# Performance work log

Hardware: AMD Instinct MI355X
Metric: run time of the kernel (lower is better)

The kernel has to match this reference:

```python
import jax, jax.numpy as jnp
import numpy as np

HEADS = 16


def setup_inputs() -> dict:
    key0 = jax.random.key(0)
    ks = jax.random.split(key0, 12)
    B, S, H = 4, 2048, 1024
    init = lambda k, shape: (jax.random.normal(k, shape, dtype=jnp.float32) * 0.02)
    return {
        "key": jax.random.normal(ks[0], (B, S, H), dtype=jnp.float32),
        "query": jax.random.normal(ks[1], (B, S, H), dtype=jnp.float32),
        "value": jax.random.normal(ks[2], (B, S, H), dtype=jnp.float32),
        "mask": jnp.zeros((B, 1, S, S), dtype=jnp.float32),  # additive mask
        "wq": init(ks[3], (H, H)), "bq": jnp.zeros((H,), jnp.float32),
        "wk": init(ks[4], (H, H)), "bk": jnp.zeros((H,), jnp.float32),
        "wv": init(ks[5], (H, H)), "bv": jnp.zeros((H,), jnp.float32),
        "wo": init(ks[6], (H, H)), "bo": jnp.zeros((H,), jnp.float32),
    }


def reference(key, query, value, mask, wq, bq, wk, bk, wv, bv, wo, bo):
    B, S, H = query.shape
    Hs = H // HEADS
    # Linear projections (torch Linear: x @ W^T + b), split heads -> [B, Hn, S, Hs]
    split = lambda x: x.reshape(B, S, HEADS, Hs).transpose(0, 2, 1, 3)
    q = split(query @ wq.T + bq)
    k = split(key @ wk.T + bk)
    v = split(value @ wv.T + bv)
    scale = 1.0 / jnp.sqrt(jnp.asarray(Hs, q.dtype))
    scores = jnp.einsum("bhqd,bhkd->bhqk", q, k) * scale  # [B, Hn, S, S]
    probs = jax.nn.softmax(scores + mask, axis=-1)  # dropout p=0 -> identity
    ctx = jnp.einsum("bhqk,bhkd->bhqd", probs, v)
    ctx = ctx.transpose(0, 2, 1, 3).reshape(B, S, H)
    return ctx @ wo.T + bo
```

## Files before the change

kernel.cpp:

```cpp
#include <hip/hip_runtime.h>
#include <hip/hip_bf16.h>

typedef __bf16 bf16;
typedef __bf16 bf16x4 __attribute__((ext_vector_type(4)));
typedef __bf16 bf16x8 __attribute__((ext_vector_type(8)));
typedef float f32x4 __attribute__((ext_vector_type(4)));
typedef float f32x16 __attribute__((ext_vector_type(16)));
typedef unsigned u32x4 __attribute__((ext_vector_type(4)));

#define MFMA16(a, b, c) __builtin_amdgcn_mfma_f32_16x16x32_bf16((a), (b), (c), 0, 0, 0)
#define MFMA32(a, b, c) __builtin_amdgcn_mfma_f32_32x32x16_bf16((a), (b), (c), 0, 0, 0)

__device__ __forceinline__ int xcd_swizzle(int bid, int nblk) {
  const int per = nblk >> 3;
  return (bid & 7) * per + (bid >> 3);
}

__device__ __forceinline__ void gload_lds16(const bf16* g, bf16* lds) {
  __builtin_amdgcn_global_load_lds(
      (const __attribute__((address_space(1))) void*)g,
      (__attribute__((address_space(3))) void*)lds, 16, 0, 0);
}

__device__ __forceinline__ float fast_exp2(float x) {
  float r;
  asm("v_exp_f32 %0, %1\n\ts_nop 1" : "=v"(r) : "v"(x));
  return r;
}

__device__ __forceinline__ unsigned cvt_pk_bf16(float lo, float hi) {
  unsigned r;
  asm("v_cvt_pk_bf16_f32 %0, %1, %2" : "=v"(r) : "v"(lo), "v"(hi));
  return r;
}

template <typename T> struct StageRegs;
template <> struct StageRegs<float> { float4 lo[2], hi[2]; };
template <> struct StageRegs<bf16> { bf16x8 v[2]; };

template <typename T>
__device__ __forceinline__ void stage_issue(StageRegs<T>& r, const T* base,
                                            int brc, int k0, int tid) {
#pragma unroll
  for (int i = 0; i < 2; ++i) {
    const int c = i * 256 + tid;
    const int row = c >> 2, lin = c & 3;
    const T* p = base + (size_t)(brc + row) * 1024 + k0 + lin * 8;
    if constexpr (sizeof(T) == 4) {
      r.lo[i] = *reinterpret_cast<const float4*>(p);
      r.hi[i] = *reinterpret_cast<const float4*>(p + 4);
    } else {
      r.v[i] = *reinterpret_cast<const bf16x8*>(p);
    }
  }
}

template <typename T>
__device__ __forceinline__ void stage_write(const StageRegs<T>& r, bf16* sm,
                                            int tid) {
#pragma unroll
  for (int i = 0; i < 2; ++i) {
    const int c = i * 256 + tid;
    const int row = c >> 2, lin = c & 3;
    const int slot = lin ^ (row & 3);
    if constexpr (sizeof(T) == 4) {
      const float4 a = r.lo[i], b = r.hi[i];
      u32x4 w;
      w[0] = cvt_pk_bf16(a.x, a.y);
      w[1] = cvt_pk_bf16(a.z, a.w);
      w[2] = cvt_pk_bf16(b.x, b.y);
      w[3] = cvt_pk_bf16(b.z, b.w);
      *reinterpret_cast<u32x4*>(sm + row * 32 + slot * 8) = w;
    } else {
      *reinterpret_cast<bf16x8*>(sm + row * 32 + slot * 8) = r.v[i];
    }
  }
}

template <typename TA>
__device__ __forceinline__ void gemm_core(const TA* A, const float* W,
                                          int brow, int bcol, int tid, int wm,
                                          int wn, int l15, int l4,
                                          bf16 (*Asm)[4096], bf16 (*Bsm)[4096],
                                          f32x4 (&acc)[4][4]) {
  StageRegs<TA> ra;
  StageRegs<float> rb;
  stage_issue(ra, A, brow, 0, tid);
  stage_issue(rb, W, bcol, 0, tid);
  int p = 0;
  for (int t = 0; t < 32; ++t) {
    stage_write(ra, Asm[p], tid);
    stage_write(rb, Bsm[p], tid);
    __syncthreads();
    if (t + 1 < 32) {
      stage_issue(ra, A, brow, (t + 1) << 5, tid);
      stage_issue(rb, W, bcol, (t + 1) << 5, tid);
    }
    bf16x8 af[4], bfr[4];
#pragma unroll
    for (int m = 0; m < 4; ++m) {
      const int row = wm + m * 16 + l15;
      const int slot = l4 ^ (row & 3);
      af[m] = *reinterpret_cast<const bf16x8*>(Asm[p] + row * 32 + slot * 8);
    }
#pragma unroll
    for (int n = 0; n < 4; ++n) {
      const int row = wn + n * 16 + l15;
      const int slot = l4 ^ (row & 3);
      bfr[n] = *reinterpret_cast<const bf16x8*>(Bsm[p] + row * 32 + slot * 8);
    }
    __builtin_amdgcn_s_setprio(1);
#pragma unroll
    for (int m = 0; m < 4; ++m)
#pragma unroll
      for (int n = 0; n < 4; ++n)
        acc[m][n] = MFMA16(af[m], bfr[n], acc[m][n]);
    __builtin_amdgcn_s_setprio(0);
    p ^= 1;
  }
}

__global__ __launch_bounds__(256, 2) void qkv_gemm_kernel(
    const float* __restrict__ query, const float* __restrict__ key,
    const float* __restrict__ value, const float* __restrict__ wq,
    const float* __restrict__ wk, const float* __restrict__ wv,
    const float* __restrict__ bq, const float* __restrict__ bk,
    const float* __restrict__ bv, bf16* __restrict__ Qws,
    bf16* __restrict__ Kws, bf16* __restrict__ Vt, float qscale) {
  __shared__ bf16 Asm[2][128 * 32];
  __shared__ bf16 Bsm[2][128 * 32];
  const int tid = threadIdx.x;
  const int lane = tid & 63;
  const int wid = tid >> 6;
  const int l15 = lane & 15;
  const int l4 = lane >> 4;
  const int bid = xcd_swizzle(blockIdx.x, 1536);
  const int seg = bid / 512;
  const int inner = bid % 512;
  const int brow = (inner >> 3) << 7;
  const int bcol = (inner & 7) << 7;
  const int wm = (wid >> 1) << 6;
  const int wn = (wid & 1) << 6;

  const float* A = seg == 0 ? query : (seg == 1 ? key : value);
  const float* W = seg == 0 ? wq : (seg == 1 ? wk : wv);
  const float* bias = seg == 0 ? bq : (seg == 1 ? bk : bv);

  f32x4 acc[4][4] = {};
  gemm_core(A, W, brow, bcol, tid, wm, wn, l15, l4, Asm, Bsm, acc);

  const int r0 = brow + wm + l4 * 4;
  const int c0 = bcol + wn + l15;
  if (seg < 2) {
    bf16* C = seg == 0 ? Qws : Kws;
    const float cs = seg == 0 ? qscale : 1.0f;
#pragma unroll
    for (int n = 0; n < 4; ++n) {
      const float bvv = bias[c0 + n * 16];
#pragma unroll
      for (int m = 0; m < 4; ++m)
#pragma unroll
        for (int r = 0; r < 4; ++r)
          C[(size_t)(r0 + m * 16 + r) * 1024 + (c0 + n * 16)] =
              (bf16)((acc[m][n][r] + bvv) * cs);
    }
  } else {
#pragma unroll
    for (int n = 0; n < 4; ++n) {
      const float bvv = bias[c0 + n * 16];
      const int col = c0 + n * 16;
#pragma unroll
      for (int m = 0; m < 4; ++m) {
        const int row = r0 + m * 16;
        const int bq_ = row >> 11;
        const int srow = row & 2047;
        uint2 w;
        w.x = cvt_pk_bf16(acc[m][n][0] + bvv, acc[m][n][1] + bvv);
        w.y = cvt_pk_bf16(acc[m][n][2] + bvv, acc[m][n][3] + bvv);
        *reinterpret_cast<uint2*>(
            &Vt[(size_t)(bq_ * 1024 + col) * 2048 + srow]) = w;
      }
    }
  }
}

__global__ __launch_bounds__(256, 2) void out_gemm_kernel(
    const bf16* __restrict__ A, const float* __restrict__ W,
    const float* __restrict__ bias, float* __restrict__ C) {
  __shared__ bf16 Asm[2][128 * 32];
  __shared__ bf16 Bsm[2][128 * 32];
  const int tid = threadIdx.x;
  const int lane = tid & 63;
  const int wid = tid >> 6;
  const int l15 = lane & 15;
  const int l4 = lane >> 4;
  const int bid = xcd_swizzle(blockIdx.x, 512);
  const int brow = (bid >> 3) << 7;
  const int bcol = (bid & 7) << 7;
  const int wm = (wid >> 1) << 6;
  const int wn = (wid & 1) << 6;

  f32x4 acc[4][4] = {};
  gemm_core(A, W, brow, bcol, tid, wm, wn, l15, l4, Asm, Bsm, acc);

  const int r0 = brow + wm + l4 * 4;
  const int c0 = bcol + wn + l15;
#pragma unroll
  for (int n = 0; n < 4; ++n) {
    const float bvv = bias[c0 + n * 16];
#pragma unroll
    for (int m = 0; m < 4; ++m)
#pragma unroll
      for (int r = 0; r < 4; ++r)
        C[(size_t)(r0 + m * 16 + r) * 1024 + (c0 + n * 16)] =
            acc[m][n][r] + bvv;
  }
}

__global__ __launch_bounds__(256) void prep_mask_kernel(
    const float* __restrict__ mask, bf16* __restrict__ M2) {
  const float LOG2E = 1.44269504088896f;
  const int T0 = blockIdx.x * 256 + threadIdx.x;
#pragma unroll
  for (int i = 0; i < 4; ++i) {
    const int O = T0 + i * 524288;
    const int a = O & 3;
    const int h5 = (O >> 2) & 1;
    const int q = (O >> 3) & 2047;
    const int t = (O >> 14) & 31;
    const int b = O >> 19;
    const float* src = mask + ((size_t)(b * 2048 + q)) * 2048 + t * 64 +
                       32 * (a >> 1) + 16 * (a & 1) + 8 * h5;
    const float4 x = *reinterpret_cast<const float4*>(src);
    const float4 y = *reinterpret_cast<const float4*>(src + 4);
    u32x4 w;
    w[0] = cvt_pk_bf16(x.x * LOG2E, x.y * LOG2E);
    w[1] = cvt_pk_bf16(x.z * LOG2E, x.w * LOG2E);
    w[2] = cvt_pk_bf16(y.x * LOG2E, y.y * LOG2E);
    w[3] = cvt_pk_bf16(y.z * LOG2E, y.w * LOG2E);
    *reinterpret_cast<u32x4*>(&M2[(size_t)O * 8]) = w;
  }
}

__global__ __launch_bounds__(256, 3) void attn_kernel(
    const bf16* __restrict__ Q, const bf16* __restrict__ Kt,
    const bf16* __restrict__ Vt, const bf16* __restrict__ M2,
    bf16* __restrict__ ctx) {
  __shared__ bf16 Ksm[2][64 * 64];
  __shared__ bf16 Vsm[2][64 * 64];
  const int lid = xcd_swizzle(blockIdx.x, 1024);
  const int h = lid & 15;
  const int qb = (lid >> 4) & 15;
  const int b = lid >> 8;
  const int tid = threadIdx.x;
  const int lane = tid & 63;
  const int wid = tid >> 6;
  const int l31 = lane & 31;
  const int h5 = lane >> 5;
  const int qbase = qb * 128 + wid * 32;

  bf16x8 qf[4];
#pragma unroll
  for (int c = 0; c < 4; ++c)
    qf[c] = *reinterpret_cast<const bf16x8*>(
        &Q[(size_t)(b * 2048 + qbase + l31) * 1024 + h * 64 + c * 16 + h5 * 8]);

  f32x16 o[2] = {};
  float lrow = 0.f;

  const bf16* Kb = Kt + (size_t)b * 2048 * 1024 + h * 64;
  const bf16* Vb = Vt + (size_t)(b * 16 + h) * 64 * 2048;

  const int ca = tid, cb = 256 + tid;
  const int ra_ = ca >> 3, la = (ca & 7) ^ (ra_ & 7);
  const int rb_ = cb >> 3, lb = (cb & 7) ^ (rb_ & 7);
  const int pra = (ra_ & 51) | ((ra_ & 4) << 1) | ((ra_ & 8) >> 1);
  const int prb = (rb_ & 51) | ((rb_ & 4) << 1) | ((rb_ & 8) >> 1);
  const bf16* kga = Kb + (size_t)pra * 1024 + la * 8;
  const bf16* kgb = Kb + (size_t)prb * 1024 + lb * 8;
  const bf16* vga = Vb + (size_t)ra_ * 2048 + la * 8;
  const bf16* vgb = Vb + (size_t)rb_ * 2048 + lb * 8;
  const bf16* mp =
      M2 + ((size_t)(b * 32) * 2048 + qbase + l31) * 64 + h5 * 32;

  auto stage = [&](int p) {
    gload_lds16(kga, &Ksm[p][tid * 8]);
    gload_lds16(kgb, &Ksm[p][2048 + tid * 8]);
    gload_lds16(vga, &Vsm[p][tid * 8]);
    gload_lds16(vgb, &Vsm[p][2048 + tid * 8]);
    kga += 64 * 1024; kgb += 64 * 1024;
    vga += 64; vgb += 64;
  };
  u32x4 mA[4], mB[4];
  auto load_mask = [&](u32x4(&mr)[4]) {
#pragma unroll
    for (int i = 0; i < 4; ++i)
      mr[i] = *reinterpret_cast<const u32x4*>(mp + i * 8);
    mp += 2048 * 64;
  };

  auto tile_compute = [&](int p, u32x4(&mr)[4]) {
    f32x16 sf[2];
#pragma unroll
    for (int w = 0; w < 16; ++w) {
      const unsigned word = mr[w >> 2][w & 3];
      const int s = w >> 3;
      const int base = ((w >> 1) & 3) * 4 + (w & 1) * 2;
      sf[s][base + 0] = __builtin_bit_cast(float, word << 16);
      sf[s][base + 1] = __builtin_bit_cast(float, word & 0xffff0000u);
    }

    __builtin_amdgcn_s_setprio(1);
#pragma unroll
    for (int s = 0; s < 2; ++s) {
#pragma unroll
      for (int c = 0; c < 4; ++c) {
        const int row = s * 32 + l31;
        const int slot = (2 * c + h5) ^ (row & 7);
        const bf16x8 kf =
            *reinterpret_cast<const bf16x8*>(&Ksm[p][row * 64 + slot * 8]);
        sf[s] = MFMA32(kf, qf[c], sf[s]);
      }
    }
    __builtin_amdgcn_s_setprio(0);

    unsigned pk[2][4][2];
#pragma unroll
    for (int s = 0; s < 2; ++s) {
#pragma unroll
      for (int g = 0; g < 4; ++g) {
        const float p0 = fast_exp2(sf[s][g * 4 + 0]);
        const float p1 = fast_exp2(sf[s][g * 4 + 1]);
        const float p2 = fast_exp2(sf[s][g * 4 + 2]);
        const float p3 = fast_exp2(sf[s][g * 4 + 3]);
        lrow += (p0 + p1) + (p2 + p3);
        pk[s][g][0] = cvt_pk_bf16(p0, p1);
        pk[s][g][1] = cvt_pk_bf16(p2, p3);
      }
    }

    __builtin_amdgcn_s_setprio(1);
#pragma unroll
    for (int c = 0; c < 4; ++c) {
      const int s = c >> 1;
      const int g0 = 2 * (c & 1);
      const u32x4 uu = {pk[s][g0][0], pk[s][g0][1], pk[s][g0 + 1][0],
                        pk[s][g0 + 1][1]};
      const bf16x8 pa = __builtin_bit_cast(bf16x8, uu);
#pragma unroll
      for (int dsub = 0; dsub < 2; ++dsub) {
        const int row = dsub * 32 + l31;
        const int slot = (2 * c + h5) ^ (row & 7);
        const bf16x8 vf =
            *reinterpret_cast<const bf16x8*>(&Vsm[p][row * 64 + slot * 8]);
        o[dsub] = MFMA32(pa, vf, o[dsub]);
      }
    }
    __builtin_amdgcn_s_setprio(0);
  };

  stage(0);
  load_mask(mA);

  for (int t = 0; t < 32; t += 2) {
    if (t + 1 < 32) {
      stage(1);
      load_mask(mB);
      asm volatile("s_waitcnt vmcnt(8)" ::: "memory");
    } else {
      asm volatile("s_waitcnt vmcnt(0)" ::: "memory");
    }
    __builtin_amdgcn_s_barrier();
    __builtin_amdgcn_sched_barrier(0);
    tile_compute(0, mA);
    __builtin_amdgcn_s_barrier();
    if (t + 2 < 32) {
      stage(0);
      load_mask(mA);
      asm volatile("s_waitcnt vmcnt(8)" ::: "memory");
    } else {
      asm volatile("s_waitcnt vmcnt(0)" ::: "memory");
    }
    __builtin_amdgcn_s_barrier();
    __builtin_amdgcn_sched_barrier(0);
    tile_compute(1, mB);
    __builtin_amdgcn_s_barrier();
  }

  lrow += __shfl_xor(lrow, 32, 64);
  const float linv = __builtin_amdgcn_rcpf(lrow);
#pragma unroll
  for (int reg = 0; reg < 16; ++reg) {
    const int qr = (reg & 3) + 8 * (reg >> 2) + 4 * h5;
    const float li = __shfl(linv, qr, 64);
    const int q = qbase + qr;
#pragma unroll
    for (int dsub = 0; dsub < 2; ++dsub) {
      ctx[(size_t)(b * 2048 + q) * 1024 + h * 64 + dsub * 32 + l31] =
          (bf16)(o[dsub][reg] * li);
    }
  }
}

extern "C" void kernel_launch(void* const* d_in, const int* in_sizes, int n_in,
                              void* d_out, int out_size, void* d_ws,
                              size_t ws_size, hipStream_t stream) {
  const float* key = (const float*)d_in[0];
  const float* query = (const float*)d_in[1];
  const float* value = (const float*)d_in[2];
  const float* mask = (const float*)d_in[3];
  const float* wq = (const float*)d_in[4];
  const float* bq = (const float*)d_in[5];
  const float* wk = (const float*)d_in[6];
  const float* bk = (const float*)d_in[7];
  const float* wv = (const float*)d_in[8];
  const float* bv = (const float*)d_in[9];
  const float* wo = (const float*)d_in[10];
  const float* bo = (const float*)d_in[11];
  float* out = (float*)d_out;

  const size_t NBSH = (size_t)4 * 2048 * 1024;
  bf16* Qws = (bf16*)d_ws;
  bf16* Kws = Qws + NBSH;
  bf16* Vt = Kws + NBSH;
  bf16* M2 = (bf16*)d_out;

  prep_mask_kernel<<<2048, dim3(256), 0, stream>>>(mask, M2);
  qkv_gemm_kernel<<<1536, dim3(256), 0, stream>>>(query, key, value, wq, wk,
                                                  wv, bq, bk, bv, Qws, Kws, Vt,
                                                  0.18033688011112f);
  attn_kernel<<<1024, dim3(256), 0, stream>>>(Qws, Kws, Vt, M2, Qws);
  out_gemm_kernel<<<512, dim3(256), 0, stream>>>(Qws, wo, bo, out);
}
```

Baseline: 259.0 us.

## Pre-convert QKV inputs and weights to bf16 and use direct-to-LDS GEMM

Fuses fp32-to-bf16 conversion of query/key/value and the three projection weights into the mask prep kernel. A new QKV GEMM then streams the bf16 operands straight into LDS with global_load_lds, instead of reading fp32 and converting inside the GEMM. This cuts the bytes the GEMM reads and drops the in-loop conversion. In exchange it adds an extra pass that writes and rereads the activations, and it needs a larger workspace, falling back to the old path when the workspace is too small.

```diff
diff --git a/kernel.cpp b/kernel.cpp
--- a/kernel.cpp
+++ b/kernel.cpp
@@ -117,6 +117,42 @@
         acc[m][n] = MFMA16(af[m], bfr[n], acc[m][n]);
     __builtin_amdgcn_s_setprio(0);
     p ^= 1;
+  }
+}
+
+__device__ __forceinline__ void qkv_epilogue(
+    int seg, const float* bias, f32x4 (&acc)[4][4], int r0, int c0,
+    bf16* Qws, bf16* Kws, bf16* Vt, float qscale) {
+  if (seg < 2) {
+    bf16* C = seg == 0 ? Qws : Kws;
+    const float cs = seg == 0 ? qscale : 1.0f;
+#pragma unroll
+    for (int n = 0; n < 4; ++n) {
+      const float bvv = bias[c0 + n * 16];
+#pragma unroll
+      for (int m = 0; m < 4; ++m)
+#pragma unroll
+        for (int r = 0; r < 4; ++r)
+          C[(size_t)(r0 + m * 16 + r) * 1024 + (c0 + n * 16)] =
+              (bf16)((acc[m][n][r] + bvv) * cs);
+    }
+  } else {
+#pragma unroll
+    for (int n = 0; n < 4; ++n) {
+      const float bvv = bias[c0 + n * 16];
+      const int col = c0 + n * 16;
+#pragma unroll
+      for (int m = 0; m < 4; ++m) {
+        const int row = r0 + m * 16;
+        const int bq_ = row >> 11;
+        const int srow = row & 2047;
+        uint2 w;
+        w.x = cvt_pk_bf16(acc[m][n][0] + bvv, acc[m][n][1] + bvv);
+        w.y = cvt_pk_bf16(acc[m][n][2] + bvv, acc[m][n][3] + bvv);
+        *reinterpret_cast<uint2*>(
+            &Vt[(size_t)(bq_ * 1024 + col) * 2048 + srow]) = w;
+      }
+    }
   }
 }
 
@@ -148,40 +184,87 @@
 
   f32x4 acc[4][4] = {};
   gemm_core(A, W, brow, bcol, tid, wm, wn, l15, l4, Asm, Bsm, acc);
-
-  const int r0 = brow + wm + l4 * 4;
-  const int c0 = bcol + wn + l15;
-  if (seg < 2) {
-    bf16* C = seg == 0 ? Qws : Kws;
-    const float cs = seg == 0 ? qscale : 1.0f;
+  qkv_epilogue(seg, bias, acc, brow + wm + l4 * 4, bcol + wn + l15, Qws, Kws,
+               Vt, qscale);
+}
+
+__global__ __launch_bounds__(256, 2) void qkv_gemm_bf16_kernel(
+    const bf16* __restrict__ qbf, const bf16* __restrict__ kbf,
+    const bf16* __restrict__ vbf, const bf16* __restrict__ wqb,
+    const bf16* __restrict__ wkb, const bf16* __restrict__ wvb,
+    const float* __restrict__ bq, const float* __restrict__ bk,
+    const float* __restrict__ bv, bf16* __restrict__ Qws,
+    bf16* __restrict__ Kws, bf16* __restrict__ Vt, float qscale) {
+  __shared__ bf16 Asm[2][128 * 32];
+  __shared__ bf16 Bsm[2][128 * 32];
+  const int tid = threadIdx.x;
+  const int lane = tid & 63;
+  const int wid = tid >> 6;
+  const int l15 = lane & 15;
+  const int l4 = lane >> 4;
+  const int bid = xcd_swizzle(blockIdx.x, 1536);
+  const int seg = bid / 512;
+  const int inner = bid % 512;
+  const int brow = (inner >> 3) << 7;
+  const int bcol = (inner & 7) << 7;
+  const int wm = (wid >> 1) << 6;
+  const int wn = (wid & 1) << 6;
+
+  const bf16* A = seg == 0 ? qbf : (seg == 1 ? kbf : vbf);
+  const bf16* W = seg == 0 ? wqb : (seg == 1 ? wkb : wvb);
+  const float* bias = seg == 0 ? bq : (seg == 1 ? bk : bv);
+
+  const int c0_ = tid, c1_ = 256 + tid;
+  const int r0s = c0_ >> 2, s0s = ((c0_ & 3) ^ (r0s & 3)) * 8;
+  const int r1s = c1_ >> 2, s1s = ((c1_ & 3) ^ (r1s & 3)) * 8;
+  const bf16* ga0 = A + (size_t)(brow + r0s) * 1024 + s0s;
+  const bf16* ga1 = A + (size_t)(brow + r1s) * 1024 + s1s;
+  const bf16* gb0 = W + (size_t)(bcol + r0s) * 1024 + s0s;
+  const bf16* gb1 = W + (size_t)(bcol + r1s) * 1024 + s1s;
+
+  f32x4 acc[4][4] = {};
+  int p = 0;
+  gload_lds16(ga0, &Asm[0][tid * 8]);
+  gload_lds16(ga1, &Asm[0][2048 + tid * 8]);
+  gload_lds16(gb0, &Bsm[0][tid * 8]);
+  gload_lds16(gb1, &Bsm[0][2048 + tid * 8]);
+  ga0 += 32; ga1 += 32; gb0 += 32; gb1 += 32;
+
+  for (int t = 0; t < 32; ++t) {
+    asm volatile("s_waitcnt vmcnt(0)" ::: "memory");
+    __builtin_amdgcn_s_barrier();
+    __builtin_amdgcn_sched_barrier(0);
+    if (t + 1 < 32) {
+      gload_lds16(ga0, &Asm[p ^ 1][tid * 8]);
+      gload_lds16(ga1, &Asm[p ^ 1][2048 + tid * 8]);
+      gload_lds16(gb0, &Bsm[p ^ 1][tid * 8]);
+      gload_lds16(gb1, &Bsm[p ^ 1][2048 + tid * 8]);
+      ga0 += 32; ga1 += 32; gb0 += 32; gb1 += 32;
+    }
+    bf16x8 af[4], bfr[4];
+#pragma unroll
+    for (int m = 0; m < 4; ++m) {
+      const int row = wm + m * 16 + l15;
+      const int slot = l4 ^ (row & 3);
+      af[m] = *reinterpret_cast<const bf16x8*>(Asm[p] + row * 32 + slot * 8);
+    }
 #pragma unroll
     for (int n = 0; n < 4; ++n) {
-      const float bvv = bias[c0 + n * 16];
-#pragma unroll
-      for (int m = 0; m < 4; ++m)
-#pragma unroll
-        for (int r = 0; r < 4; ++r)
-          C[(size_t)(r0 + m * 16 + r) * 1024 + (c0 + n * 16)] =
-              (bf16)((acc[m][n][r] + bvv) * cs);
-    }
-  } else {
-#pragma unroll
-    for (int n = 0; n < 4; ++n) {
-      const float bvv = bias[c0 + n * 16];
-      const int col = c0 + n * 16;
-#pragma unroll
-      for (int m = 0; m < 4; ++m) {
-        const int row = r0 + m * 16;
-        const int bq_ = row >> 11;
-        const int srow = row & 2047;
-        uint2 w;
-        w.x = cvt_pk_bf16(acc[m][n][0] + bvv, acc[m][n][1] + bvv);
-        w.y = cvt_pk_bf16(acc[m][n][2] + bvv, acc[m][n][3] + bvv);
-        *reinterpret_cast<uint2*>(
-            &Vt[(size_t)(bq_ * 1024 + col) * 2048 + srow]) = w;
-      }
-    }
-  }
+      const int row = wn + n * 16 + l15;
+      const int slot = l4 ^ (row & 3);
+      bfr[n] = *reinterpret_cast<const bf16x8*>(Bsm[p] + row * 32 + slot * 8);
+    }
+    __builtin_amdgcn_s_setprio(1);
+#pragma unroll
+    for (int m = 0; m < 4; ++m)
+#pragma unroll
+      for (int n = 0; n < 4; ++n)
+        acc[m][n] = MFMA16(af[m], bfr[n], acc[m][n]);
+    __builtin_amdgcn_s_setprio(0);
+    p ^= 1;
+  }
+  qkv_epilogue(seg, bias, acc, brow + wm + l4 * 4, bcol + wn + l15, Qws, Kws,
+               Vt, qscale);
 }
 
 __global__ __launch_bounds__(256, 2) void out_gemm_kernel(
@@ -217,8 +300,14 @@
   }
 }
 
-__global__ __launch_bounds__(256) void prep_mask_kernel(
-    const float* __restrict__ mask, bf16* __restrict__ M2) {
+__global__ __launch_bounds__(256) void prep_kernel(
+    const float* __restrict__ mask, bf16* __restrict__ M2,
+    const float* __restrict__ query, const float* __restrict__ key,
+    const float* __restrict__ value, const float* __restrict__ wq,
+    const float* __restrict__ wk, const float* __restrict__ wv,
+    bf16* __restrict__ qbf, bf16* __restrict__ kbf, bf16* __restrict__ vbf,
+    bf16* __restrict__ wqb, bf16* __restrict__ wkb, bf16* __restrict__ wvb,
+    int do_conv) {
   const float LOG2E = 1.44269504088896f;
   const int T0 = blockIdx.x * 256 + threadIdx.x;
 #pragma unroll
@@ -240,6 +329,38 @@
     w[3] = cvt_pk_bf16(y.z * LOG2E, y.w * LOG2E);
     *reinterpret_cast<u32x4*>(&M2[(size_t)O * 8]) = w;
   }
+  if (do_conv) {
+#pragma unroll
+    for (int i = 0; i < 6; ++i) {
+      const int u = T0 + i * 524288;
+      const int seg = u >> 20;
+      const size_t off = (size_t)(u & 1048575) * 8;
+      const float* s = (seg == 0 ? query : (seg == 1 ? key : value)) + off;
+      bf16* d = (seg == 0 ? qbf : (seg == 1 ? kbf : vbf)) + off;
+      const float4 x = *reinterpret_cast<const float4*>(s);
+      const float4 y = *reinterpret_cast<const float4*>(s + 4);
+      u32x4 w;
+      w[0] = cvt_pk_bf16(x.x, x.y);
+      w[1] = cvt_pk_bf16(x.z, x.w);
+      w[2] = cvt_pk_bf16(y.x, y.y);
+      w[3] = cvt_pk_bf16(y.z, y.w);
+      *reinterpret_cast<u32x4*>(d) = w;
+    }
+    if (T0 < 393216) {
+      const int seg = T0 >> 17;
+      const size_t off = (size_t)(T0 & 131071) * 8;
+      const float* s = (seg == 0 ? wq : (seg == 1 ? wk : wv)) + off;
+      bf16* d = (seg == 0 ? wqb : (seg == 1 ? wkb : wvb)) + off;
+      const float4 x = *reinterpret_cast<const float4*>(s);
+      const float4 y = *reinterpret_cast<const float4*>(s + 4);
+      u32x4 w;
+      w[0] = cvt_pk_bf16(x.x, x.y);
+      w[1] = cvt_pk_bf16(x.z, x.w);
+      w[2] = cvt_pk_bf16(y.x, y.y);
+      w[3] = cvt_pk_bf16(y.z, y.w);
+      *reinterpret_cast<u32x4*>(d) = w;
+    }
+  }
 }
 
 __global__ __launch_bounds__(256, 3) void attn_kernel(
@@ -423,12 +544,28 @@
   bf16* Qws = (bf16*)d_ws;
   bf16* Kws = Qws + NBSH;
   bf16* Vt = Kws + NBSH;
+  bf16* qbf = Qws + 3 * NBSH;
+  bf16* kbf = Qws + 4 * NBSH;
+  bf16* vbf = Qws + 5 * NBSH;
+  bf16* wqb = Qws + 6 * NBSH;
+  bf16* wkb = wqb + 1048576;
+  bf16* wvb = wkb + 1048576;
   bf16* M2 = (bf16*)d_out;
 
-  prep_mask_kernel<<<2048, dim3(256), 0, stream>>>(mask, M2);
-  qkv_gemm_kernel<<<1536, dim3(256), 0, stream>>>(query, key, value, wq, wk,
-                                                  wv, bq, bk, bv, Qws, Kws, Vt,
-                                                  0.18033688011112f);
+  const bool conv = ws_size >= (size_t)106954752;
+
+  prep_kernel<<<2048, dim3(256), 0, stream>>>(
+      mask, M2, query, key, value, wq, wk, wv, qbf, kbf, vbf, wqb, wkb, wvb,
+      conv ? 1 : 0);
+  if (conv) {
+    qkv_gemm_bf16_kernel<<<1536, dim3(256), 0, stream>>>(
+        qbf, kbf, vbf, wqb, wkb, wvb, bq, bk, bv, Qws, Kws, Vt,
+        0.18033688011112f);
+  } else {
+    qkv_gemm_kernel<<<1536, dim3(256), 0, stream>>>(
+        query, key, value, wq, wk, wv, bq, bk, bv, Qws, Kws, Vt,
+        0.18033688011112f);
+  }
   attn_kernel<<<1024, dim3(256), 0, stream>>>(Qws, Kws, Vt, M2, Qws);
   out_gemm_kernel<<<512, dim3(256), 0, stream>>>(Qws, wo, bo, out);
 }
```

Result: slower. 272.7 us (+5.3%).
